# Kernel optimization log

Measured on AMD Instinct MI355X. Metric: run time of the kernel, lower is better.

## Reference

```python
import jax, jax.numpy as jnp
import numpy as np
import math

B, S, HID, NH = 2, 1024, 4096, 32
HD = HID // NH  # 128


def setup_inputs() -> dict:
    key = jax.random.key(0)
    ks = jax.random.split(key, 6)
    scale = 0.02
    x = jax.random.normal(ks[0], (B, S, HID), dtype=jnp.float32)
    Wq = jax.random.normal(ks[1], (HID, HID), dtype=jnp.float32) * scale
    Wk = jax.random.normal(ks[2], (HID, HID), dtype=jnp.float32) * scale
    Wv = jax.random.normal(ks[3], (HID, HID), dtype=jnp.float32) * scale
    Wo = jax.random.normal(ks[4], (HID, HID), dtype=jnp.float32) * scale
    bq = jnp.zeros((HID,), jnp.float32)
    bk = jnp.zeros((HID,), jnp.float32)
    bv = jnp.zeros((HID,), jnp.float32)
    bo = jnp.zeros((HID,), jnp.float32)
    position_ids = jnp.tile(jnp.arange(S, dtype=jnp.int32)[None, :], (B, 1))
    # additive causal mask: 0 on/below diagonal, large negative above
    causal = jnp.tril(jnp.ones((S, S), dtype=bool))
    attention_mask = jnp.where(causal, 0.0, -1e9).astype(jnp.float32)[None, None]
    return {"x": x, "Wq": Wq, "bq": bq, "Wk": Wk, "bk": bk, "Wv": Wv,
            "bv": bv, "Wo": Wo, "bo": bo, "position_ids": position_ids,
            "attention_mask": attention_mask}


def _rotate_interleaved(t):
    # stack([-t[..., 1::2], t[..., ::2]], -1).reshape_as(t)
    return jnp.stack([-t[..., 1::2], t[..., ::2]], axis=-1).reshape(t.shape)


def reference(x, Wq, bq, Wk, bk, Wv, bv, Wo, bo, position_ids, attention_mask):
    b, s, _ = x.shape
    q = x @ Wq.T + bq
    k = x @ Wk.T + bk
    v = x @ Wv.T + bv
    # [B, NH, S, HD]
    q = q.reshape(b, s, NH, HD).transpose(0, 2, 1, 3)
    k = k.reshape(b, s, NH, HD).transpose(0, 2, 1, 3)
    v = v.reshape(b, s, NH, HD).transpose(0, 2, 1, 3)
    # RoPE (interleaved pairs), cos/sin recomputed each call as in source
    inv_freq = 1.0 / (10000.0 ** (jnp.arange(0, HD, 2, dtype=jnp.float32) / HD))
    ang = position_ids.astype(jnp.float32)[..., None] * inv_freq  # [B,S,HD/2]
    cos = jnp.repeat(jnp.cos(ang), 2, axis=-1)[:, None]  # [B,1,S,HD]
    sin = jnp.repeat(jnp.sin(ang), 2, axis=-1)[:, None]
    q = q * cos + _rotate_interleaved(q) * sin
    k = k * cos + _rotate_interleaved(k) * sin
    # naive full attention
    scores = jnp.einsum('bhqd,bhkd->bhqk', q, k) / math.sqrt(HD)
    scores = scores + attention_mask
    probs = jax.nn.softmax(scores, axis=-1)
    out = jnp.einsum('bhqk,bhkd->bhqd', probs, v)
    out = out.transpose(0, 2, 1, 3).reshape(b, s, HID)
    return out @ Wo.T + bo
```

## Files before the change

### kernel.cpp

```cpp
#include <hip/hip_runtime.h>
#include <hip/hip_bf16.h>
#include <cmath>

constexpr int cB  = 2;
constexpr int cS  = 1024;
constexpr int cNH = 32;
constexpr int cHD = 128;
constexpr int cHID = 4096;
constexpr int cM  = cB * cS;

typedef unsigned short u16;
typedef __bf16 bf16x8 __attribute__((ext_vector_type(8)));
typedef float  f32x4  __attribute__((ext_vector_type(4)));

__device__ __forceinline__ u16 f2b(float f) { return __builtin_bit_cast(u16, (__bf16)f); }

__global__ void cvt_bf16(const float* __restrict__ in, u16* __restrict__ out, int n8) {
  int i = blockIdx.x * blockDim.x + threadIdx.x;
  if (i >= n8) return;
  const float4* in4 = (const float4*)in;
  float4 a = in4[2 * i], b = in4[2 * i + 1];
  union { u16 u[8]; uint4 v; } r;
  r.u[0] = f2b(a.x); r.u[1] = f2b(a.y); r.u[2] = f2b(a.z); r.u[3] = f2b(a.w);
  r.u[4] = f2b(b.x); r.u[5] = f2b(b.y); r.u[6] = f2b(b.z); r.u[7] = f2b(b.w);
  ((uint4*)out)[i] = r.v;
}

__global__ void cvt3(const float* __restrict__ A0, const float* __restrict__ A1,
                     const float* __restrict__ A2,
                     u16* __restrict__ O0, u16* __restrict__ O1, u16* __restrict__ O2) {
  int idx = blockIdx.x * blockDim.x + threadIdx.x;
  int sel = idx >> 21, t = idx & ((1 << 21) - 1);
  const float* in = (sel == 0) ? A0 : (sel == 1 ? A1 : A2);
  u16* out = (sel == 0) ? O0 : (sel == 1 ? O1 : O2);
  const float4* in4 = (const float4*)in;
  float4 a = in4[2 * t], b = in4[2 * t + 1];
  union { u16 u[8]; uint4 v; } rv;
  rv.u[0] = f2b(a.x); rv.u[1] = f2b(a.y); rv.u[2] = f2b(a.z); rv.u[3] = f2b(a.w);
  rv.u[4] = f2b(b.x); rv.u[5] = f2b(b.y); rv.u[6] = f2b(b.z); rv.u[7] = f2b(b.w);
  ((uint4*)out)[t] = rv.v;
}

__global__ void rope_table_k(const int* __restrict__ pos,
                             float* __restrict__ cosT, float* __restrict__ sinT) {
  int idx = blockIdx.x * blockDim.x + threadIdx.x;
  int i = idx & 63, bs = idx >> 6;
  float p = (float)pos[bs];
  float freq = exp2f(-(float)i * (13.287712379549449f / 64.0f));
  float a = p * freq;
  float s, c;
  sincosf(a, &s, &c);
  cosT[idx] = c; sinT[idx] = s;
}

__global__ void rope_apply(u16* __restrict__ Q, u16* __restrict__ Kb,
                           const float* __restrict__ cosT, const float* __restrict__ sinT) {
  int idx = blockIdx.x * blockDim.x + threadIdx.x;
  const int nPer = cB * cS * cNH * (cHD / 8);
  u16* P = (idx < nPer) ? Q : Kb;
  int t = (idx < nPer) ? idx : idx - nPer;
  int d8 = t & 15;
  int h  = (t >> 4) & 31;
  int bs = t >> 9;
  size_t base = ((size_t)bs * cNH + h) * cHD + d8 * 8;
  uint4 v = *reinterpret_cast<uint4*>(P + base);
  u16* u = reinterpret_cast<u16*>(&v);
  int pb = bs * 64 + d8 * 4;
  float4 cs = *reinterpret_cast<const float4*>(cosT + pb);
  float4 sn = *reinterpret_cast<const float4*>(sinT + pb);
  float co[4] = {cs.x, cs.y, cs.z, cs.w};
  float si[4] = {sn.x, sn.y, sn.z, sn.w};
#pragma unroll
  for (int p = 0; p < 4; ++p) {
    float e = (float)__builtin_bit_cast(__bf16, u[2 * p]);
    float o = (float)__builtin_bit_cast(__bf16, u[2 * p + 1]);
    float e2 = e * co[p] - o * si[p];
    float o2 = o * co[p] + e * si[p];
    u[2 * p]     = f2b(e2);
    u[2 * p + 1] = f2b(o2);
  }
  *reinterpret_cast<uint4*>(P + base) = v;
}

__global__ void transpose_v(const u16* __restrict__ V, u16* __restrict__ Vt) {
  __shared__ u16 tile[32][33];
  int bh = blockIdx.z;
  int b = bh >> 5, h = bh & 31;
  int s0 = blockIdx.x * 32, d0 = blockIdx.y * 32;
  int tx = threadIdx.x & 31, ty0 = threadIdx.x >> 5;
#pragma unroll
  for (int i = 0; i < 4; ++i) {
    int r = ty0 + i * 8;
    tile[r][tx] = V[((size_t)(b * cS + s0 + r) * cNH + h) * cHD + d0 + tx];
  }
  __syncthreads();
#pragma unroll
  for (int i = 0; i < 4; ++i) {
    int r = ty0 + i * 8;
    Vt[((size_t)bh * cHD + d0 + r) * cS + s0 + tx] = tile[tx][r];
  }
}

template <int MODE>
__global__ __launch_bounds__(512, 2)
void gemm8(const u16* __restrict__ A,
           const u16* __restrict__ W0, const u16* __restrict__ W1,
           const u16* __restrict__ W2,
           const float* __restrict__ b0, const float* __restrict__ b1,
           const float* __restrict__ b2,
           void* o0, void* o1, void* o2,
           const float* __restrict__ cosT, const float* __restrict__ sinT) {
  __shared__ __align__(16) u16 sA[3][128 * 64];
  __shared__ __align__(16) u16 sB[3][256 * 64];
  const int tid = threadIdx.x;
  const int wid = tid >> 6, lane = tid & 63;
  const int c = lane & 15, g = lane >> 4;
  const int wm = wid >> 2, wn = wid & 3;
  const int m0 = blockIdx.x * 128;
  const int gn0 = blockIdx.y * 256;
  const int sel = gn0 >> 12;
  const int n0 = gn0 & 4095;
  const u16* Bw = (sel == 0) ? W0 : (sel == 1 ? W1 : W2);

  f32x4 acc[4][4] = {};
  const int nkt = cHID / 64;

#define STAGE_A(kt, dst)                                                       \
  {                                                                            \
    _Pragma("unroll") for (int l = 0; l < 2; ++l) {                            \
      int chunk = (l * 8 + wid) * 64 + lane;                                   \
      int row = chunk >> 3, kc = (chunk & 7) ^ (row & 7);                      \
      __builtin_amdgcn_global_load_lds(                                        \
          (const void*)(A + (size_t)(m0 + row) * cHID + (kt) * 64 + kc * 8),   \
          (void*)(&sA[dst][(l * 8 + wid) * 512]), 16, 0, 0);                   \
    }                                                                          \
  }
#define STAGE_B(kt, dst)                                                       \
  {                                                                            \
    _Pragma("unroll") for (int l = 0; l < 4; ++l) {                            \
      int chunk = (l * 8 + wid) * 64 + lane;                                   \
      int row = chunk >> 3, kc = (chunk & 7) ^ (row & 7);                      \
      __builtin_amdgcn_global_load_lds(                                        \
          (const void*)(Bw + (size_t)(n0 + row) * cHID + (kt) * 64 + kc * 8),  \
          (void*)(&sB[dst][(l * 8 + wid) * 512]), 16, 0, 0);                   \
    }                                                                          \
  }

  STAGE_A(0, 0); STAGE_B(0, 0);
  STAGE_A(1, 1); STAGE_B(1, 1);
  asm volatile("s_waitcnt vmcnt(6)" ::: "memory");
  __builtin_amdgcn_sched_barrier(0);
  __builtin_amdgcn_s_barrier();
  asm volatile("" ::: "memory");
  __builtin_amdgcn_sched_barrier(0);

  for (int kt = 0; kt < nkt; ++kt) {
    const int bufR = kt % 3;
    const int bufW = (kt + 2) % 3;
    const bool doStage = (kt + 2) < nkt;

    bf16x8 af[4], bw[4];
#pragma unroll
    for (int mf = 0; mf < 4; ++mf) {
      int ra = wm * 64 + mf * 16 + c;
      af[mf] = *reinterpret_cast<const bf16x8*>(
          &sA[bufR][ra * 64 + ((g ^ (ra & 7)) * 8)]);
    }
#pragma unroll
    for (int nf = 0; nf < 4; ++nf) {
      int rb = wn * 64 + nf * 16 + c;
      bw[nf] = *reinterpret_cast<const bf16x8*>(
          &sB[bufR][rb * 64 + ((g ^ (rb & 7)) * 8)]);
    }
    if (doStage) STAGE_A(kt + 2, bufW);
    __builtin_amdgcn_s_setprio(1);
#pragma unroll
    for (int mf = 0; mf < 4; ++mf)
#pragma unroll
      for (int nf = 0; nf < 4; ++nf)
        acc[mf][nf] = __builtin_amdgcn_mfma_f32_16x16x32_bf16(af[mf], bw[nf], acc[mf][nf], 0, 0, 0);
    __builtin_amdgcn_s_setprio(0);

#pragma unroll
    for (int mf = 0; mf < 4; ++mf) {
      int ra = wm * 64 + mf * 16 + c;
      af[mf] = *reinterpret_cast<const bf16x8*>(
          &sA[bufR][ra * 64 + (((4 + g) ^ (ra & 7)) * 8)]);
    }
#pragma unroll
    for (int nf = 0; nf < 4; ++nf) {
      int rb = wn * 64 + nf * 16 + c;
      bw[nf] = *reinterpret_cast<const bf16x8*>(
          &sB[bufR][rb * 64 + (((4 + g) ^ (rb & 7)) * 8)]);
    }
    if (doStage) STAGE_B(kt + 2, bufW);
    __builtin_amdgcn_s_setprio(1);
#pragma unroll
    for (int mf = 0; mf < 4; ++mf)
#pragma unroll
      for (int nf = 0; nf < 4; ++nf)
        acc[mf][nf] = __builtin_amdgcn_mfma_f32_16x16x32_bf16(af[mf], bw[nf], acc[mf][nf], 0, 0, 0);
    __builtin_amdgcn_s_setprio(0);

    if (doStage) {
      asm volatile("s_waitcnt vmcnt(6)" ::: "memory");
    } else {
      asm volatile("s_waitcnt vmcnt(0)" ::: "memory");
    }
    __builtin_amdgcn_sched_barrier(0);
    __builtin_amdgcn_s_barrier();
    asm volatile("" ::: "memory");
    __builtin_amdgcn_sched_barrier(0);
  }
#undef STAGE_A
#undef STAGE_B

  const float* bp = (sel == 0) ? b0 : (sel == 1 ? b1 : b2);
  void* op = (sel == 0) ? o0 : (sel == 1 ? o1 : o2);

  if (MODE == 0 && sel < 2) {
#pragma unroll
    for (int nf = 0; nf < 4; ++nf) {
      int col = n0 + wn * 64 + nf * 16 + c;
      float bv = bp[col];
      int ih = (((wn & 1) * 64) + nf * 16 + c) >> 1;
#pragma unroll
      for (int mf = 0; mf < 4; ++mf) {
        int row0 = m0 + wm * 64 + mf * 16 + g * 4;
#pragma unroll
        for (int r = 0; r < 4; ++r) {
          int row = row0 + r;
          float v = acc[mf][nf][r] + bv;
          float vp = __shfl_xor(v, 1);
          float cs = cosT[row * 64 + ih];
          float sn = sinT[row * 64 + ih];
          v = (c & 1) ? fmaf(vp, sn, v * cs)
                      : fmaf(-vp, sn, v * cs);
          ((u16*)op)[(size_t)row * cHID + col] = f2b(v);
        }
      }
    }
  } else if (MODE == 0) {
    u16* vt = (u16*)op;
#pragma unroll
    for (int nf = 0; nf < 4; ++nf) {
      int col = n0 + wn * 64 + nf * 16 + c;
      float bv = bp[col];
      int hh = col >> 7, dd = col & 127;
#pragma unroll
      for (int mf = 0; mf < 4; ++mf) {
        int row0 = m0 + wm * 64 + mf * 16 + g * 4;
        int bb = row0 >> 10, sl = row0 & 1023;
        ushort4 pk;
        pk.x = f2b(acc[mf][nf][0] + bv);
        pk.y = f2b(acc[mf][nf][1] + bv);
        pk.z = f2b(acc[mf][nf][2] + bv);
        pk.w = f2b(acc[mf][nf][3] + bv);
        *reinterpret_cast<ushort4*>(
            vt + ((size_t)(bb * cNH + hh) * cHD + dd) * cS + sl) = pk;
      }
    }
  } else {
#pragma unroll
    for (int nf = 0; nf < 4; ++nf) {
      int col = n0 + wn * 64 + nf * 16 + c;
      float bv = bp[col];
#pragma unroll
      for (int mf = 0; mf < 4; ++mf) {
        int row = m0 + wm * 64 + mf * 16 + g * 4;
#pragma unroll
        for (int r = 0; r < 4; ++r) {
          float v = acc[mf][nf][r] + bv;
          if (MODE == 1)
            ((float*)op)[(size_t)(row + r) * cHID + col] = v;
          else
            ((u16*)op)[(size_t)(row + r) * cHID + col] = f2b(v);
        }
      }
    }
  }
}

__global__ __launch_bounds__(256, 2)
void attn_kernel(const u16* __restrict__ Q, const u16* __restrict__ Kb,
                 const u16* __restrict__ Vt, u16* __restrict__ O) {
  __shared__ __align__(16) char sK[2][16384];
  __shared__ __align__(16) char sP[8192];
  const int tid = threadIdx.x, w = tid >> 6, lane = tid & 63;
  const int c = lane & 15, g = lane >> 4;
  const int bh = blockIdx.y;
  const int b = bh >> 5, h = bh & 31;
  const int NT = cS / 64;
  const int qtA = blockIdx.x, qtB = NT - 1 - blockIdx.x;
  const float kSc = 0.12751744f;
  const u16* Vg = Vt + (size_t)bh * (cHD * cS);

  bf16x8 qf[2][4];
#pragma unroll
  for (int s = 0; s < 2; ++s) {
    int q0s = (s ? qtA : qtB) * 64;
    size_t qrow = ((size_t)(b * cS + q0s + w * 16 + c) * cNH + h) * cHD;
#pragma unroll
    for (int df = 0; df < 4; ++df)
      qf[s][df] = *reinterpret_cast<const bf16x8*>(Q + qrow + df * 32 + g * 8);
  }

  f32x4 o[2][8] = {};
  float mx[2][4], ls[2][4];
#pragma unroll
  for (int s = 0; s < 2; ++s)
#pragma unroll
    for (int r = 0; r < 4; ++r) { mx[s][r] = -1e30f; ls[s][r] = 0.f; }

  uint4 kv[4];
#define LOADT(t)                                                               \
  {                                                                            \
    _Pragma("unroll") for (int i = 0; i < 4; ++i) {                            \
      int cidx = i * 256 + tid;                                                \
      int row = cidx >> 4, ch = cidx & 15;                                     \
      kv[i] = *reinterpret_cast<const uint4*>(                                 \
          Kb + ((size_t)(b * cS + (t) * 64 + row) * cNH + h) * cHD + ch * 8);  \
    }                                                                          \
  }
#define WRITET(buf)                                                            \
  {                                                                            \
    _Pragma("unroll") for (int i = 0; i < 4; ++i) {                            \
      int cidx = i * 256 + tid;                                                \
      int row = cidx >> 4, ch = cidx & 15;                                     \
      *reinterpret_cast<uint4*>(sK[buf] + row * 256 + ((ch ^ (row & 7)) * 16)) = kv[i]; \
    }                                                                          \
  }

  LOADT(0);
  WRITET(0);
  int cur = 0;

  for (int t = 0; t <= qtB; ++t) {
    __syncthreads();
    if (t < qtB) LOADT(t + 1);

#pragma unroll
    for (int s = 0; s < 2; ++s) {
      const int qt_s = s ? qtA : qtB;
      if (t > qt_s) continue;
      const int q0_s = qt_s * 64;

      f32x4 sc[4] = {};
#pragma unroll
      for (int df = 0; df < 4; ++df) {
        bf16x8 kb[4];
#pragma unroll
        for (int cf = 0; cf < 4; ++cf) {
          int kr = cf * 16 + c;
          kb[cf] = *reinterpret_cast<const bf16x8*>(sK[cur] + kr * 256 + (((df * 4 + g) ^ (kr & 7)) * 16));
        }
#pragma unroll
        for (int cf = 0; cf < 4; ++cf)
          sc[cf] = __builtin_amdgcn_mfma_f32_16x16x32_bf16(qf[s][df], kb[cf], sc[cf], 0, 0, 0);
      }

      if (t == qt_s) {
#pragma unroll
        for (int cf = 0; cf < 4; ++cf) {
          int kg = t * 64 + cf * 16 + c;
#pragma unroll
          for (int r = 0; r < 4; ++r) {
            int qg = q0_s + w * 16 + g * 4 + r;
            if (kg > qg) sc[cf][r] = -1e30f;
          }
        }
      }

      float alpha[4];
#pragma unroll
      for (int r = 0; r < 4; ++r) {
        float v = fmaxf(fmaxf(sc[0][r], sc[1][r]), fmaxf(sc[2][r], sc[3][r]));
        v = fmaxf(v, __shfl_xor(v, 1));
        v = fmaxf(v, __shfl_xor(v, 2));
        v = fmaxf(v, __shfl_xor(v, 4));
        v = fmaxf(v, __shfl_xor(v, 8));
        float mn = fmaxf(mx[s][r], v);
        alpha[r] = exp2f((mx[s][r] - mn) * kSc);
        mx[s][r] = mn;
      }
      float rs[4] = {0.f, 0.f, 0.f, 0.f};
#pragma unroll
      for (int cf = 0; cf < 4; ++cf)
#pragma unroll
        for (int r = 0; r < 4; ++r) {
          float p = exp2f((sc[cf][r] - mx[s][r]) * kSc);
          sc[cf][r] = p;
          rs[r] += p;
        }
#pragma unroll
      for (int r = 0; r < 4; ++r) {
        float v = rs[r];
        v += __shfl_xor(v, 1); v += __shfl_xor(v, 2);
        v += __shfl_xor(v, 4); v += __shfl_xor(v, 8);
        ls[s][r] = ls[s][r] * alpha[r] + v;
      }
#pragma unroll
      for (int nf = 0; nf < 8; ++nf)
#pragma unroll
        for (int r = 0; r < 4; ++r)
          o[s][nf][r] *= alpha[r];

      char* myP = sP + w * 2048;
#pragma unroll
      for (int cf = 0; cf < 4; ++cf) {
        int kcol = cf * 16 + c;
        int chunk = kcol >> 3, within = kcol & 7;
#pragma unroll
        for (int r = 0; r < 4; ++r) {
          int qr = g * 4 + r;
          *reinterpret_cast<u16*>(myP + qr * 128 + ((chunk ^ (qr & 7)) * 16) + within * 2) =
              f2b(sc[cf][r]);
        }
      }
      bf16x8 pa[2];
#pragma unroll
      for (int kf = 0; kf < 2; ++kf)
        pa[kf] = *reinterpret_cast<const bf16x8*>(myP + c * 128 + (((kf * 4 + g) ^ (c & 7)) * 16));

#pragma unroll
      for (int kf = 0; kf < 2; ++kf) {
        bf16x8 vb[8];
#pragma unroll
        for (int nf = 0; nf < 8; ++nf)
          vb[nf] = *reinterpret_cast<const bf16x8*>(
              Vg + (size_t)(nf * 16 + c) * cS + t * 64 + (kf * 4 + g) * 8);
#pragma unroll
        for (int nf = 0; nf < 8; ++nf)
          o[s][nf] = __builtin_amdgcn_mfma_f32_16x16x32_bf16(pa[kf], vb[nf], o[s][nf], 0, 0, 0);
      }
    }

    if (t < qtB) { WRITET(cur ^ 1); cur ^= 1; }
  }

  __syncthreads();
#pragma unroll
  for (int s = 0; s < 2; ++s) {
#pragma unroll
    for (int nf = 0; nf < 8; ++nf) {
#pragma unroll
      for (int r = 0; r < 4; ++r) {
        float v = o[s][nf][r] / ls[s][r];
        int qr = w * 16 + g * 4 + r;
        *reinterpret_cast<u16*>(sK[s] + qr * 256 + (nf * 16 + c) * 2) = f2b(v);
      }
    }
  }
  __syncthreads();
#pragma unroll
  for (int s = 0; s < 2; ++s) {
    int q0_s = (s ? qtA : qtB) * 64;
#pragma unroll
    for (int i = 0; i < 4; ++i) {
      int cidx = i * 256 + tid;
      int row = cidx >> 4, ch = cidx & 15;
      uint4 v = *reinterpret_cast<const uint4*>(sK[s] + row * 256 + ch * 16);
      *reinterpret_cast<uint4*>(O + ((size_t)(b * cS + q0_s + row) * cNH + h) * cHD + ch * 8) = v;
    }
  }
#undef LOADT
#undef WRITET
}

extern "C" void kernel_launch(void* const* d_in, const int* in_sizes, int n_in,
                              void* d_out, int out_size, void* d_ws, size_t ws_size,
                              hipStream_t stream) {
  const float* x  = (const float*)d_in[0];
  const float* Wq = (const float*)d_in[1];
  const float* bq = (const float*)d_in[2];
  const float* Wk = (const float*)d_in[3];
  const float* bk = (const float*)d_in[4];
  const float* Wv = (const float*)d_in[5];
  const float* bv = (const float*)d_in[6];
  const float* Wo = (const float*)d_in[7];
  const float* bo = (const float*)d_in[8];
  const int*  pos = (const int*)d_in[9];
  float* out = (float*)d_out;

  char* ws = (char*)d_ws;
  const size_t MB = 1u << 20;
  const int W8 = (cHID * cHID) / 8;
  const int X8 = (cM * cHID) / 8;
  const int R8 = cB * cS * cNH * (cHD / 8);

  if (ws_size >= 168 * MB) {
    u16* xb  = (u16*)(ws);
    u16* Qb  = (u16*)(ws + 16 * MB);
    u16* Kb  = (u16*)(ws + 32 * MB);
    u16* Vt  = (u16*)(ws + 48 * MB);
    float* cosT = (float*)(ws + 64 * MB);
    float* sinT = cosT + cB * cS * 64;
    u16* WbQ = (u16*)(ws + 72 * MB);
    u16* WbK = (u16*)(ws + 104 * MB);
    u16* WbV = (u16*)(ws + 136 * MB);
    u16* Ab  = WbQ;
    u16* WbO = WbK;

    cvt3<<<(3 * W8) / 256, 256, 0, stream>>>(Wq, Wk, Wv, WbQ, WbK, WbV);
    rope_table_k<<<(cB * cS * 64) / 256, 256, 0, stream>>>(pos, cosT, sinT);
    cvt_bf16<<<X8 / 256, 256, 0, stream>>>(x, xb, X8);

    gemm8<0><<<dim3(16, 48), 512, 0, stream>>>(
        xb, WbQ, WbK, WbV, bq, bk, bv, Qb, Kb, Vt, cosT, sinT);

    attn_kernel<<<dim3(cS / 128, cB * cNH), 256, 0, stream>>>(Qb, Kb, Vt, Ab);

    cvt_bf16<<<W8 / 256, 256, 0, stream>>>(Wo, WbO, W8);
    gemm8<1><<<dim3(16, 16), 512, 0, stream>>>(
        Ab, WbO, WbO, WbO, bo, bo, bo, out, out, out, nullptr, nullptr);
  } else {
    u16* xb = (u16*)(ws);
    u16* Wb = (u16*)(ws + 16 * MB);
    u16* Qb = (u16*)(ws + 48 * MB);
    u16* Kb = (u16*)(ws + 64 * MB);
    u16* Vb = (u16*)(ws + 80 * MB);
    u16* Vt = xb;
    u16* Ab = Vb;
    float* cosT = (float*)(ws + 96 * MB);
    float* sinT = cosT + cB * cS * 64;

    cvt_bf16<<<X8 / 256, 256, 0, stream>>>(x, xb, X8);
    cvt_bf16<<<W8 / 256, 256, 0, stream>>>(Wq, Wb, W8);
    gemm8<3><<<dim3(16, 16), 512, 0, stream>>>(
        xb, Wb, Wb, Wb, bq, bq, bq, Qb, Qb, Qb, nullptr, nullptr);
    cvt_bf16<<<W8 / 256, 256, 0, stream>>>(Wk, Wb, W8);
    gemm8<3><<<dim3(16, 16), 512, 0, stream>>>(
        xb, Wb, Wb, Wb, bk, bk, bk, Kb, Kb, Kb, nullptr, nullptr);
    cvt_bf16<<<W8 / 256, 256, 0, stream>>>(Wv, Wb, W8);
    gemm8<3><<<dim3(16, 16), 512, 0, stream>>>(
        xb, Wb, Wb, Wb, bv, bv, bv, Vb, Vb, Vb, nullptr, nullptr);

    rope_table_k<<<(cB * cS * 64) / 256, 256, 0, stream>>>(pos, cosT, sinT);
    rope_apply<<<(2 * R8) / 256, 256, 0, stream>>>(Qb, Kb, cosT, sinT);
    transpose_v<<<dim3(cS / 32, cHD / 32, cB * cNH), 256, 0, stream>>>(Vb, Vt);
    attn_kernel<<<dim3(cS / 128, cB * cNH), 256, 0, stream>>>(Qb, Kb, Vt, Ab);

    cvt_bf16<<<W8 / 256, 256, 0, stream>>>(Wo, Wb, W8);
    gemm8<1><<<dim3(16, 16), 512, 0, stream>>>(
        Ab, Wb, Wb, Wb, bo, bo, bo, out, out, out, nullptr, nullptr);
  }
}
```

Measured before the change: 446.5 us.

## Process one query tile per attention block instead of paired causal tiles

The attention kernel no longer pairs a short and a long causal query tile in each block. Each block now handles a single 64-row query tile, the grid is doubled, and the launch bound is raised to allow three blocks per CU. The goal is more parallelism and occupancy, and less register pressure from the duplicated accumulators. The cost is that shared K tiles are no longer reused across two query tiles, and per-block work becomes imbalanced, relying on heavy tiles being scheduled first.

```diff
diff --git a/kernel.cpp b/kernel.cpp
--- a/kernel.cpp
+++ b/kernel.cpp
@@ -281,7 +281,7 @@
   }
 }
 
-__global__ __launch_bounds__(256, 2)
+__global__ __launch_bounds__(256, 3)
 void attn_kernel(const u16* __restrict__ Q, const u16* __restrict__ Kb,
                  const u16* __restrict__ Vt, u16* __restrict__ O) {
   __shared__ __align__(16) char sK[2][16384];
@@ -291,26 +291,22 @@
   const int bh = blockIdx.y;
   const int b = bh >> 5, h = bh & 31;
   const int NT = cS / 64;
-  const int qtA = blockIdx.x, qtB = NT - 1 - blockIdx.x;
+  const int qt = NT - 1 - blockIdx.x;
+  const int q0 = qt * 64;
   const float kSc = 0.12751744f;
   const u16* Vg = Vt + (size_t)bh * (cHD * cS);
 
-  bf16x8 qf[2][4];
-#pragma unroll
-  for (int s = 0; s < 2; ++s) {
-    int q0s = (s ? qtA : qtB) * 64;
-    size_t qrow = ((size_t)(b * cS + q0s + w * 16 + c) * cNH + h) * cHD;
+  bf16x8 qf[4];
+  {
+    size_t qrow = ((size_t)(b * cS + q0 + w * 16 + c) * cNH + h) * cHD;
 #pragma unroll
     for (int df = 0; df < 4; ++df)
-      qf[s][df] = *reinterpret_cast<const bf16x8*>(Q + qrow + df * 32 + g * 8);
-  }
-
-  f32x4 o[2][8] = {};
-  float mx[2][4], ls[2][4];
-#pragma unroll
-  for (int s = 0; s < 2; ++s)
-#pragma unroll
-    for (int r = 0; r < 4; ++r) { mx[s][r] = -1e30f; ls[s][r] = 0.f; }
+      qf[df] = *reinterpret_cast<const bf16x8*>(Q + qrow + df * 32 + g * 8);
+  }
+
+  f32x4 o[8] = {};
+  float mx[4] = {-1e30f, -1e30f, -1e30f, -1e30f};
+  float ls[4] = {0.f, 0.f, 0.f, 0.f};
 
   uint4 kv[4];
 #define LOADT(t)                                                               \
@@ -335,133 +331,119 @@
   WRITET(0);
   int cur = 0;
 
-  for (int t = 0; t <= qtB; ++t) {
+  for (int t = 0; t <= qt; ++t) {
     __syncthreads();
-    if (t < qtB) LOADT(t + 1);
-
-#pragma unroll
-    for (int s = 0; s < 2; ++s) {
-      const int qt_s = s ? qtA : qtB;
-      if (t > qt_s) continue;
-      const int q0_s = qt_s * 64;
-
-      f32x4 sc[4] = {};
-#pragma unroll
-      for (int df = 0; df < 4; ++df) {
-        bf16x8 kb[4];
-#pragma unroll
-        for (int cf = 0; cf < 4; ++cf) {
-          int kr = cf * 16 + c;
-          kb[cf] = *reinterpret_cast<const bf16x8*>(sK[cur] + kr * 256 + (((df * 4 + g) ^ (kr & 7)) * 16));
+    if (t < qt) LOADT(t + 1);
+
+    f32x4 sc[4] = {};
+#pragma unroll
+    for (int df = 0; df < 4; ++df) {
+      bf16x8 kb[4];
+#pragma unroll
+      for (int cf = 0; cf < 4; ++cf) {
+        int kr = cf * 16 + c;
+        kb[cf] = *reinterpret_cast<const bf16x8*>(sK[cur] + kr * 256 + (((df * 4 + g) ^ (kr & 7)) * 16));
+      }
+#pragma unroll
+      for (int cf = 0; cf < 4; ++cf)
+        sc[cf] = __builtin_amdgcn_mfma_f32_16x16x32_bf16(qf[df], kb[cf], sc[cf], 0, 0, 0);
+    }
+
+    if (t == qt) {
+#pragma unroll
+      for (int cf = 0; cf < 4; ++cf) {
+        int kg = t * 64 + cf * 16 + c;
+#pragma unroll
+        for (int r = 0; r < 4; ++r) {
+          int qg = q0 + w * 16 + g * 4 + r;
+          if (kg > qg) sc[cf][r] = -1e30f;
         }
-#pragma unroll
-        for (int cf = 0; cf < 4; ++cf)
-          sc[cf] = __builtin_amdgcn_mfma_f32_16x16x32_bf16(qf[s][df], kb[cf], sc[cf], 0, 0, 0);
-      }
-
-      if (t == qt_s) {
-#pragma unroll
-        for (int cf = 0; cf < 4; ++cf) {
-          int kg = t * 64 + cf * 16 + c;
-#pragma unroll
-          for (int r = 0; r < 4; ++r) {
-            int qg = q0_s + w * 16 + g * 4 + r;
-            if (kg > qg) sc[cf][r] = -1e30f;
-          }
-        }
-      }
-
-      float alpha[4];
+      }
+    }
+
+    float alpha[4];
+#pragma unroll
+    for (int r = 0; r < 4; ++r) {
+      float v = fmaxf(fmaxf(sc[0][r], sc[1][r]), fmaxf(sc[2][r], sc[3][r]));
+      v = fmaxf(v, __shfl_xor(v, 1));
+      v = fmaxf(v, __shfl_xor(v, 2));
+      v = fmaxf(v, __shfl_xor(v, 4));
+      v = fmaxf(v, __shfl_xor(v, 8));
+      float mn = fmaxf(mx[r], v);
+      alpha[r] = exp2f((mx[r] - mn) * kSc);
+      mx[r] = mn;
+    }
+    float rs[4] = {0.f, 0.f, 0.f, 0.f};
+#pragma unroll
+    for (int cf = 0; cf < 4; ++cf)
 #pragma unroll
       for (int r = 0; r < 4; ++r) {
-        float v = fmaxf(fmaxf(sc[0][r], sc[1][r]), fmaxf(sc[2][r], sc[3][r]));
-        v = fmaxf(v, __shfl_xor(v, 1));
-        v = fmaxf(v, __shfl_xor(v, 2));
-        v = fmaxf(v, __shfl_xor(v, 4));
-        v = fmaxf(v, __shfl_xor(v, 8));
-        float mn = fmaxf(mx[s][r], v);
-        alpha[r] = exp2f((mx[s][r] - mn) * kSc);
-        mx[s][r] = mn;
-      }
-      float rs[4] = {0.f, 0.f, 0.f, 0.f};
-#pragma unroll
-      for (int cf = 0; cf < 4; ++cf)
-#pragma unroll
-        for (int r = 0; r < 4; ++r) {
-          float p = exp2f((sc[cf][r] - mx[s][r]) * kSc);
-          sc[cf][r] = p;
-          rs[r] += p;
-        }
+        float p = exp2f((sc[cf][r] - mx[r]) * kSc);
+        sc[cf][r] = p;
+        rs[r] += p;
+      }
+#pragma unroll
+    for (int r = 0; r < 4; ++r) {
+      float v = rs[r];
+      v += __shfl_xor(v, 1); v += __shfl_xor(v, 2);
+      v += __shfl_xor(v, 4); v += __shfl_xor(v, 8);
+      ls[r] = ls[r] * alpha[r] + v;
+    }
+#pragma unroll
+    for (int nf = 0; nf < 8; ++nf)
+#pragma unroll
+      for (int r = 0; r < 4; ++r)
+        o[nf][r] *= alpha[r];
+
+    char* myP = sP + w * 2048;
+#pragma unroll
+    for (int cf = 0; cf < 4; ++cf) {
+      int kcol = cf * 16 + c;
+      int chunk = kcol >> 3, within = kcol & 7;
 #pragma unroll
       for (int r = 0; r < 4; ++r) {
-        float v = rs[r];
-        v += __shfl_xor(v, 1); v += __shfl_xor(v, 2);
-        v += __shfl_xor(v, 4); v += __shfl_xor(v, 8);
-        ls[s][r] = ls[s][r] * alpha[r] + v;
-      }
+        int qr = g * 4 + r;
+        *reinterpret_cast<u16*>(myP + qr * 128 + ((chunk ^ (qr & 7)) * 16) + within * 2) =
+            f2b(sc[cf][r]);
+      }
+    }
+    bf16x8 pa[2];
+#pragma unroll
+    for (int kf = 0; kf < 2; ++kf)
+      pa[kf] = *reinterpret_cast<const bf16x8*>(myP + c * 128 + (((kf * 4 + g) ^ (c & 7)) * 16));
+
+#pragma unroll
+    for (int kf = 0; kf < 2; ++kf) {
+      bf16x8 vb[8];
 #pragma unroll
       for (int nf = 0; nf < 8; ++nf)
-#pragma unroll
-        for (int r = 0; r < 4; ++r)
-          o[s][nf][r] *= alpha[r];
-
-      char* myP = sP + w * 2048;
-#pragma unroll
-      for (int cf = 0; cf < 4; ++cf) {
-        int kcol = cf * 16 + c;
-        int chunk = kcol >> 3, within = kcol & 7;
-#pragma unroll
-        for (int r = 0; r < 4; ++r) {
-          int qr = g * 4 + r;
-          *reinterpret_cast<u16*>(myP + qr * 128 + ((chunk ^ (qr & 7)) * 16) + within * 2) =
-              f2b(sc[cf][r]);
-        }
-      }
-      bf16x8 pa[2];
-#pragma unroll
-      for (int kf = 0; kf < 2; ++kf)
-        pa[kf] = *reinterpret_cast<const bf16x8*>(myP + c * 128 + (((kf * 4 + g) ^ (c & 7)) * 16));
-
-#pragma unroll
-      for (int kf = 0; kf < 2; ++kf) {
-        bf16x8 vb[8];
-#pragma unroll
-        for (int nf = 0; nf < 8; ++nf)
-          vb[nf] = *reinterpret_cast<const bf16x8*>(
-              Vg + (size_t)(nf * 16 + c) * cS + t * 64 + (kf * 4 + g) * 8);
-#pragma unroll
-        for (int nf = 0; nf < 8; ++nf)
-          o[s][nf] = __builtin_amdgcn_mfma_f32_16x16x32_bf16(pa[kf], vb[nf], o[s][nf], 0, 0, 0);
-      }
-    }
-
-    if (t < qtB) { WRITET(cur ^ 1); cur ^= 1; }
+        vb[nf] = *reinterpret_cast<const bf16x8*>(
+            Vg + (size_t)(nf * 16 + c) * cS + t * 64 + (kf * 4 + g) * 8);
+#pragma unroll
+      for (int nf = 0; nf < 8; ++nf)
+        o[nf] = __builtin_amdgcn_mfma_f32_16x16x32_bf16(pa[kf], vb[nf], o[nf], 0, 0, 0);
+    }
+
+    if (t < qt) { WRITET(cur ^ 1); cur ^= 1; }
   }
 
   __syncthreads();
 #pragma unroll
-  for (int s = 0; s < 2; ++s) {
-#pragma unroll
-    for (int nf = 0; nf < 8; ++nf) {
-#pragma unroll
-      for (int r = 0; r < 4; ++r) {
-        float v = o[s][nf][r] / ls[s][r];
-        int qr = w * 16 + g * 4 + r;
-        *reinterpret_cast<u16*>(sK[s] + qr * 256 + (nf * 16 + c) * 2) = f2b(v);
-      }
+  for (int nf = 0; nf < 8; ++nf) {
+#pragma unroll
+    for (int r = 0; r < 4; ++r) {
+      float v = o[nf][r] / ls[r];
+      int qr = w * 16 + g * 4 + r;
+      *reinterpret_cast<u16*>(sK[0] + qr * 256 + (nf * 16 + c) * 2) = f2b(v);
     }
   }
   __syncthreads();
 #pragma unroll
-  for (int s = 0; s < 2; ++s) {
-    int q0_s = (s ? qtA : qtB) * 64;
-#pragma unroll
-    for (int i = 0; i < 4; ++i) {
-      int cidx = i * 256 + tid;
-      int row = cidx >> 4, ch = cidx & 15;
-      uint4 v = *reinterpret_cast<const uint4*>(sK[s] + row * 256 + ch * 16);
-      *reinterpret_cast<uint4*>(O + ((size_t)(b * cS + q0_s + row) * cNH + h) * cHD + ch * 8) = v;
-    }
+  for (int i = 0; i < 4; ++i) {
+    int cidx = i * 256 + tid;
+    int row = cidx >> 4, ch = cidx & 15;
+    uint4 v = *reinterpret_cast<const uint4*>(sK[0] + row * 256 + ch * 16);
+    *reinterpret_cast<uint4*>(O + ((size_t)(b * cS + q0 + row) * cNH + h) * cHD + ch * 8) = v;
   }
 #undef LOADT
 #undef WRITET
@@ -508,7 +490,7 @@
     gemm8<0><<<dim3(16, 48), 512, 0, stream>>>(
         xb, WbQ, WbK, WbV, bq, bk, bv, Qb, Kb, Vt, cosT, sinT);
 
-    attn_kernel<<<dim3(cS / 128, cB * cNH), 256, 0, stream>>>(Qb, Kb, Vt, Ab);
+    attn_kernel<<<dim3(cS / 64, cB * cNH), 256, 0, stream>>>(Qb, Kb, Vt, Ab);
 
     cvt_bf16<<<W8 / 256, 256, 0, stream>>>(Wo, WbO, W8);
     gemm8<1><<<dim3(16, 16), 512, 0, stream>>>(
@@ -538,7 +520,7 @@
     rope_table_k<<<(cB * cS * 64) / 256, 256, 0, stream>>>(pos, cosT, sinT);
     rope_apply<<<(2 * R8) / 256, 256, 0, stream>>>(Qb, Kb, cosT, sinT);
     transpose_v<<<dim3(cS / 32, cHD / 32, cB * cNH), 256, 0, stream>>>(Vb, Vt);
-    attn_kernel<<<dim3(cS / 128, cB * cNH), 256, 0, stream>>>(Qb, Kb, Vt, Ab);
+    attn_kernel<<<dim3(cS / 64, cB * cNH), 256, 0, stream>>>(Qb, Kb, Vt, Ab);
 
     cvt_bf16<<<W8 / 256, 256, 0, stream>>>(Wo, Wb, W8);
     gemm8<1><<<dim3(16, 16), 512, 0, stream>>>(
```

After: 555.2 us. 24.3% more time.
